# Performance work log

Hardware: AMD Instinct MI355X
Metric: run time of the kernel (lower is better)

Reference implementation:

```python
import jax, jax.numpy as jnp
import numpy as np

ATTN_K = 64
H = 256  # seq_hidden_size


def setup_inputs() -> dict:
    key = jax.random.key(0)
    ks = jax.random.split(key, 10)
    N, Q = 1000000, 256
    return {
        "question": jax.random.normal(ks[0], (Q,), jnp.float32),
        "score": jax.random.uniform(ks[1], (), jnp.float32),
        "questions": jax.random.normal(ks[2], (N, Q), jnp.float32),
        "hs": jax.random.normal(ks[3], (N, H), jnp.float32),
        "W_score": jax.random.normal(ks[4], (1, Q + H), jnp.float32) * 0.05,
        "b_score": jax.random.normal(ks[5], (1,), jnp.float32) * 0.05,
        "W_ih": jax.random.normal(ks[6], (3 * H, 2 * Q), jnp.float32) * 0.05,
        "W_hh": jax.random.normal(ks[7], (3 * H, H), jnp.float32) * 0.05,
        "b_ih": jax.random.normal(ks[8], (3 * H,), jnp.float32) * 0.05,
        "b_hh": jax.random.normal(ks[9], (3 * H,), jnp.float32) * 0.05,
    }


def reference(question, score, questions, hs, W_score, b_score, W_ih, W_hh, b_ih, b_hh):
    # Attention over history: dot-product scores, top-k, softmax-weighted sum.
    alpha = questions @ question                      # [N]
    vals, idx = jax.lax.top_k(alpha, ATTN_K)          # [k], [k]
    w = jax.nn.softmax(vals)                          # softmax over the k selected scores
    attn_h = w @ hs[idx]                              # [H] weighted gather-sum

    # Score head on [question ; attn_h]
    pred_v = jnp.concatenate([question, attn_h])      # [Q+H]
    pred = W_score @ pred_v + b_score                 # [1]

    # GRU input: question gated by correctness of score
    right = (score >= 0.5).astype(question.dtype)
    x = jnp.concatenate([question * right, question * (1.0 - right)])  # [2Q]

    # Single GRU step (PyTorch gate ordering: r, z, n)
    h = hs[-1]                                        # [H]
    gx = W_ih @ x + b_ih                              # [3H]
    gh = W_hh @ h + b_hh                              # [3H]
    xr, xz, xn = gx[:H], gx[H:2 * H], gx[2 * H:]
    hr, hz, hn = gh[:H], gh[H:2 * H], gh[2 * H:]
    r = jax.nn.sigmoid(xr + hr)
    z = jax.nn.sigmoid(xz + hz)
    n = jnp.tanh(xn + r * hn)
    h_new = (1.0 - z) * n + z * h                     # [H]
    return pred, h_new
```

## Files before the change

### kernel.cpp

```cpp
#include <hip/hip_runtime.h>
#include <math.h>

#define Q 256
#define H 256
#define ATTN_K 64
#define CAP 4096
#define HBINS 4096
#define NREP 8

typedef float f4 __attribute__((ext_vector_type(4)));

__device__ __forceinline__ unsigned f2k(float f) {
    unsigned u = __float_as_uint(f);
    return u ^ ((u & 0x80000000u) ? 0xFFFFFFFFu : 0x80000000u);
}

__global__ __launch_bounds__(256) void k_prep(const float* __restrict__ question,
                                              const float* __restrict__ score,
                                              const float* __restrict__ hs,
                                              const float* __restrict__ W_ih,
                                              const float* __restrict__ W_hh,
                                              const float* __restrict__ b_ih,
                                              const float* __restrict__ b_hh,
                                              float* __restrict__ gx, float* __restrict__ gh,
                                              unsigned* __restrict__ hist,
                                              unsigned* __restrict__ state, int N) {
    const int t = threadIdx.x;
    const int b = blockIdx.x;
    const int gid = b * 256 + t;
    if (gid < NREP * HBINS) hist[gid] = 0u;
    if (gid < 16) state[gid] = 0u;

    const int lane = t & 63;
    const int o = b * 4 + (t >> 6);
    if (o >= 3 * H) return;
    const int off = (score[0] >= 0.5f) ? 0 : Q;
    const float4 q = *reinterpret_cast<const float4*>(question + lane * 4);
    const float4 h = *reinterpret_cast<const float4*>(hs + (size_t)(N - 1) * H + lane * 4);
    const float4 wx = *reinterpret_cast<const float4*>(W_ih + (size_t)o * (2 * Q) + off + lane * 4);
    const float4 wh = *reinterpret_cast<const float4*>(W_hh + (size_t)o * H + lane * 4);
    float px = wx.x * q.x + wx.y * q.y + wx.z * q.z + wx.w * q.w;
    float ph = wh.x * h.x + wh.y * h.y + wh.z * h.z + wh.w * h.w;
#pragma unroll
    for (int d = 32; d > 0; d >>= 1) {
        px += __shfl_xor(px, d, 64);
        ph += __shfl_xor(ph, d, 64);
    }
    if (lane == 0) {
        gx[o] = px + b_ih[o];
        gh[o] = ph + b_hh[o];
    }
}

__global__ __launch_bounds__(256, 8) void k_main(const float* __restrict__ questions,
                                                 const float* __restrict__ question,
                                                 unsigned* __restrict__ hist,
                                                 float* __restrict__ alpha, int N) {
    __shared__ unsigned hb[HBINS];
    const int t = threadIdx.x;
    const int b = blockIdx.x;
#pragma unroll
    for (int j = 0; j < HBINS / 256; ++j) hb[t + j * 256] = 0u;
    __syncthreads();

    const int lane = t & 63;
    const int sub = lane & 15;
    const int rg  = lane >> 4;
    const int wid = b * 4 + (t >> 6);
    const int nw  = (gridDim.x * blockDim.x) >> 6;

    float4 q[4];
#pragma unroll
    for (int j = 0; j < 4; ++j)
        q[j] = *reinterpret_cast<const float4*>(question + j * 64 + sub * 4);

    const size_t stepRows = (size_t)nw * 8;
    const float* baseA = questions + ((size_t)wid * 8 + rg) * Q + sub * 4;
    for (size_t r0 = (size_t)wid * 8; r0 < (size_t)N; r0 += stepRows, baseA += stepRows * Q) {
        const int rA = (int)r0 + rg;
        const int rB = rA + 4;
        float pA = 0.f, pB = 0.f;
        if (rA < N) {
#pragma unroll
            for (int j = 0; j < 4; ++j) {
                f4 x = __builtin_nontemporal_load(reinterpret_cast<const f4*>(baseA + j * 64));
                pA = fmaf(x.x, q[j].x, fmaf(x.y, q[j].y, fmaf(x.z, q[j].z, fmaf(x.w, q[j].w, pA))));
            }
        }
        if (rB < N) {
#pragma unroll
            for (int j = 0; j < 4; ++j) {
                f4 x = __builtin_nontemporal_load(reinterpret_cast<const f4*>(baseA + 4 * Q + j * 64));
                pB = fmaf(x.x, q[j].x, fmaf(x.y, q[j].y, fmaf(x.z, q[j].z, fmaf(x.w, q[j].w, pB))));
            }
        }
#pragma unroll
        for (int d = 1; d < 16; d <<= 1) {
            pA += __shfl_xor(pA, d, 64);
            pB += __shfl_xor(pB, d, 64);
        }
        if (sub == 0) {
            if (rA < N) {
                alpha[rA] = pA;
                int rel = (int)(f2k(pA) >> 19) - 4096;
                if (rel >= 0) atomicAdd(&hb[rel], 1u);
            }
            if (rB < N) {
                alpha[rB] = pB;
                int rel = (int)(f2k(pB) >> 19) - 4096;
                if (rel >= 0) atomicAdd(&hb[rel], 1u);
            }
        }
    }

    __syncthreads();
    const unsigned rep = (unsigned)(b & (NREP - 1)) << 12;
#pragma unroll
    for (int j = 0; j < HBINS / 256; ++j) {
        unsigned v = hb[t + j * 256];
        if (v) atomicAdd(&hist[rep + t + j * 256], v);
    }
}

__global__ __launch_bounds__(256) void k_select(const float* __restrict__ alpha,
                                                const float* __restrict__ question,
                                                const float* __restrict__ hs,
                                                const float* __restrict__ W_score,
                                                const float* __restrict__ b_score,
                                                const unsigned* __restrict__ hist,
                                                unsigned* __restrict__ state,
                                                float* __restrict__ cval, int* __restrict__ cidx,
                                                const float* __restrict__ gx,
                                                const float* __restrict__ gh,
                                                float* __restrict__ out, int N) {
    __shared__ float lv[CAP];
    __shared__ int li[CAP];
    __shared__ float sw[ATTN_K];
    __shared__ int si[ATTN_K];
    __shared__ float red[256];
    __shared__ unsigned wsum[4];
    __shared__ int tau_sh;
    __shared__ int last_sh;
    const int t = threadIdx.x;
    const int lane = t & 63;
    const int w = t >> 6;

    unsigned c[16];
    {
        const int base16 = 4080 - 16 * t;
#pragma unroll
        for (int g = 0; g < 16; ++g) c[g] = 0u;
#pragma unroll
        for (int r = 0; r < NREP; ++r) {
            const uint4* h4 = reinterpret_cast<const uint4*>(hist + (r << 12) + base16);
#pragma unroll
            for (int k = 0; k < 4; ++k) {
                uint4 v = h4[k];
                c[4 * k + 0] += v.x; c[4 * k + 1] += v.y;
                c[4 * k + 2] += v.z; c[4 * k + 3] += v.w;
            }
        }
    }
    unsigned tsum = 0;
#pragma unroll
    for (int g = 0; g < 16; ++g) tsum += c[g];
    unsigned cum = tsum;
#pragma unroll
    for (int d = 1; d < 64; d <<= 1) {
        unsigned y = __shfl_up(cum, d, 64);
        if (lane >= d) cum += y;
    }
    if (lane == 63) wsum[w] = cum;
    __syncthreads();
    {
        unsigned add = 0;
        for (int i = 0; i < w; ++i) add += wsum[i];
        cum += add;
    }
    const unsigned before = cum - tsum;
    if (cum >= (unsigned)ATTN_K && before < (unsigned)ATTN_K) {
        unsigned acc = before;
        int taub = 4080 - 16 * t;
        for (int g = 15; g >= 0; --g) {
            acc += c[g];
            if (acc >= (unsigned)ATTN_K) { taub = 4080 - 16 * t + g; break; }
        }
        tau_sh = taub;
    }
    if (t == 255 && cum < (unsigned)ATTN_K) tau_sh = 0;
    __syncthreads();
    const int tau = tau_sh;

    {
        const int n4 = N >> 2;
        const int stride = gridDim.x * blockDim.x;
        const float4* a4 = reinterpret_cast<const float4*>(alpha);
        for (int i = blockIdx.x * blockDim.x + t; i < n4; i += stride) {
            float4 a = a4[i];
            float v[4] = {a.x, a.y, a.z, a.w};
#pragma unroll
            for (int j = 0; j < 4; ++j) {
                if ((int)(f2k(v[j]) >> 19) - 4096 >= tau) {
                    unsigned p = atomicAdd(&state[1], 1u);
                    if (p < CAP) { cval[p] = v[j]; cidx[p] = i * 4 + j; }
                }
            }
        }
        if (blockIdx.x == 0 && t < (N & 3)) {
            const int idx = (n4 << 2) + t;
            float v = alpha[idx];
            if ((int)(f2k(v) >> 19) - 4096 >= tau) {
                unsigned p = atomicAdd(&state[1], 1u);
                if (p < CAP) { cval[p] = v; cidx[p] = idx; }
            }
        }
    }

    if (t == 0) {
        __threadfence();
        last_sh = (atomicAdd(&state[2], 1u) == gridDim.x - 1) ? 1 : 0;
    }
    __syncthreads();
    if (!last_sh) return;
    __threadfence();

    const int C = min((int)state[1], CAP);
    for (int i = t; i < C; i += 256) { lv[i] = cval[i]; li[i] = cidx[i]; }
    __syncthreads();

    if (t < 64) {
        for (int k = 0; k < ATTN_K; ++k) {
            float bv = -INFINITY;
            int bi = 0x7fffffff;
            int bp = -1;
            for (int i = t; i < C; i += 64) {
                float v = lv[i];
                int id = li[i];
                if (v > bv || (v == bv && id < bi)) { bv = v; bi = id; bp = i; }
            }
#pragma unroll
            for (int d = 32; d > 0; d >>= 1) {
                float ov = __shfl_xor(bv, d, 64);
                int oi = __shfl_xor(bi, d, 64);
                int op = __shfl_xor(bp, d, 64);
                if (ov > bv || (ov == bv && oi < bi)) { bv = ov; bi = oi; bp = op; }
            }
            if (t == 0) {
                sw[k] = bv;
                si[k] = (bi == 0x7fffffff) ? 0 : bi;
                if (bp >= 0) lv[bp] = -INFINITY;
            }
        }
        float m = sw[0];
        float e = expf(sw[t] - m);
        float ssum = e;
#pragma unroll
        for (int d = 32; d > 0; d >>= 1) ssum += __shfl_xor(ssum, d, 64);
        sw[t] = e / ssum;
    }
    __syncthreads();

    float aj = 0.f;
    for (int k = 0; k < ATTN_K; ++k) {
        aj = fmaf(sw[k], hs[(size_t)si[k] * H + t], aj);
    }

    red[t] = W_score[t] * question[t] + W_score[Q + t] * aj;
    __syncthreads();
    for (int d = 128; d > 0; d >>= 1) {
        if (t < d) red[t] += red[t + d];
        __syncthreads();
    }
    if (t == 0) out[0] = red[0] + b_score[0];

    {
        float xr = gx[t], xz = gx[H + t], xn = gx[2 * H + t];
        float hr = gh[t], hz = gh[H + t], hn = gh[2 * H + t];
        float r = 1.f / (1.f + expf(-(xr + hr)));
        float z = 1.f / (1.f + expf(-(xz + hz)));
        float n = tanhf(xn + r * hn);
        float hprev = hs[(size_t)(N - 1) * H + t];
        out[1 + t] = (1.f - z) * n + z * hprev;
    }
}

extern "C" void kernel_launch(void* const* d_in, const int* in_sizes, int n_in,
                              void* d_out, int out_size, void* d_ws, size_t ws_size,
                              hipStream_t stream) {
    const float* question = (const float*)d_in[0];
    const float* score    = (const float*)d_in[1];
    const float* questions= (const float*)d_in[2];
    const float* hs       = (const float*)d_in[3];
    const float* W_score  = (const float*)d_in[4];
    const float* b_score  = (const float*)d_in[5];
    const float* W_ih     = (const float*)d_in[6];
    const float* W_hh     = (const float*)d_in[7];
    const float* b_ih     = (const float*)d_in[8];
    const float* b_hh     = (const float*)d_in[9];
    const int N = in_sizes[2] / Q;
    float* out = (float*)d_out;

    char* ws = (char*)d_ws;
    size_t off = 0;
    float* alpha = (float*)(ws + off); off += (size_t)N * sizeof(float);
    off = (off + 255) & ~(size_t)255;
    unsigned* hist = (unsigned*)(ws + off); off += (size_t)NREP * HBINS * sizeof(unsigned);
    unsigned* state = (unsigned*)(ws + off); off += 256;
    float* cval = (float*)(ws + off); off += (size_t)CAP * sizeof(float);
    int* cidx = (int*)(ws + off); off += (size_t)CAP * sizeof(int);
    float* gx = (float*)(ws + off); off += 3 * H * sizeof(float);
    float* gh = (float*)(ws + off); off += 3 * H * sizeof(float);

    k_prep<<<192, 256, 0, stream>>>(question, score, hs, W_ih, W_hh, b_ih, b_hh,
                                    gx, gh, hist, state, N);
    k_main<<<2048, 256, 0, stream>>>(questions, question, hist, alpha, N);
    k_select<<<512, 256, 0, stream>>>(alpha, question, hs, W_score, b_score, hist,
                                      state, cval, cidx, gx, gh, out, N);
}
```

Measured before the change: 243.3 us.

## Split histogram out of GEMV kernel and unroll four rows per wave

The streaming dot-product kernel no longer builds a shared-memory histogram, so it drops LDS allocation, the zeroing and merge syncs, and the per-row atomics. Each wave now handles 16 rows per iteration with four independent accumulators and no bounds checks, plus a separate tail loop, to raise memory-level parallelism. A new k_hist kernel re-reads alpha (4 MB) to build the histogram, which adds a launch and extra traffic in exchange for a leaner bandwidth-bound main loop.

After: 243.2 us. Within noise of the previous version (-0.1%).

```diff
diff --git a/kernel.cpp b/kernel.cpp
--- a/kernel.cpp
+++ b/kernel.cpp
@@ -52,21 +52,14 @@
     }
 }
 
-__global__ __launch_bounds__(256, 8) void k_main(const float* __restrict__ questions,
-                                                 const float* __restrict__ question,
-                                                 unsigned* __restrict__ hist,
-                                                 float* __restrict__ alpha, int N) {
-    __shared__ unsigned hb[HBINS];
+__global__ __launch_bounds__(256) void k_main(const float* __restrict__ questions,
+                                              const float* __restrict__ question,
+                                              float* __restrict__ alpha, int N) {
     const int t = threadIdx.x;
-    const int b = blockIdx.x;
-#pragma unroll
-    for (int j = 0; j < HBINS / 256; ++j) hb[t + j * 256] = 0u;
-    __syncthreads();
-
     const int lane = t & 63;
     const int sub = lane & 15;
     const int rg  = lane >> 4;
-    const int wid = b * 4 + (t >> 6);
+    const int wid = blockIdx.x * 4 + (t >> 6);
     const int nw  = (gridDim.x * blockDim.x) >> 6;
 
     float4 q[4];
@@ -74,51 +67,87 @@
     for (int j = 0; j < 4; ++j)
         q[j] = *reinterpret_cast<const float4*>(question + j * 64 + sub * 4);
 
-    const size_t stepRows = (size_t)nw * 8;
-    const float* baseA = questions + ((size_t)wid * 8 + rg) * Q + sub * 4;
-    for (size_t r0 = (size_t)wid * 8; r0 < (size_t)N; r0 += stepRows, baseA += stepRows * Q) {
-        const int rA = (int)r0 + rg;
-        const int rB = rA + 4;
-        float pA = 0.f, pB = 0.f;
-        if (rA < N) {
+    const int rowsPerIter = nw * 16;
+    const int B = N / rowsPerIter;
+    const float* base = questions + ((size_t)wid * 16 + rg) * Q + sub * 4;
+    for (int it = 0; it < B; ++it, base += (size_t)rowsPerIter * Q) {
+        float acc0 = 0.f, acc1 = 0.f, acc2 = 0.f, acc3 = 0.f;
+#pragma unroll
+        for (int j = 0; j < 4; ++j) {
+            f4 x0 = __builtin_nontemporal_load(reinterpret_cast<const f4*>(base + 0 * 4 * Q + j * 64));
+            f4 x1 = __builtin_nontemporal_load(reinterpret_cast<const f4*>(base + 1 * 4 * Q + j * 64));
+            f4 x2 = __builtin_nontemporal_load(reinterpret_cast<const f4*>(base + 2 * 4 * Q + j * 64));
+            f4 x3 = __builtin_nontemporal_load(reinterpret_cast<const f4*>(base + 3 * 4 * Q + j * 64));
+            acc0 = fmaf(x0.x, q[j].x, fmaf(x0.y, q[j].y, fmaf(x0.z, q[j].z, fmaf(x0.w, q[j].w, acc0))));
+            acc1 = fmaf(x1.x, q[j].x, fmaf(x1.y, q[j].y, fmaf(x1.z, q[j].z, fmaf(x1.w, q[j].w, acc1))));
+            acc2 = fmaf(x2.x, q[j].x, fmaf(x2.y, q[j].y, fmaf(x2.z, q[j].z, fmaf(x2.w, q[j].w, acc2))));
+            acc3 = fmaf(x3.x, q[j].x, fmaf(x3.y, q[j].y, fmaf(x3.z, q[j].z, fmaf(x3.w, q[j].w, acc3))));
+        }
+#pragma unroll
+        for (int d = 1; d < 16; d <<= 1) {
+            acc0 += __shfl_xor(acc0, d, 64);
+            acc1 += __shfl_xor(acc1, d, 64);
+            acc2 += __shfl_xor(acc2, d, 64);
+            acc3 += __shfl_xor(acc3, d, 64);
+        }
+        if (sub == 0) {
+            const size_t r0 = (size_t)it * rowsPerIter + (size_t)wid * 16 + rg;
+            alpha[r0]      = acc0;
+            alpha[r0 + 4]  = acc1;
+            alpha[r0 + 8]  = acc2;
+            alpha[r0 + 12] = acc3;
+        }
+    }
+
+    const int tailStart = B * rowsPerIter;
+    for (int g = wid; tailStart + g * 4 < N; g += nw) {
+        const int r = tailStart + g * 4 + rg;
+        float p = 0.f;
+        if (r < N) {
+            const float* row = questions + (size_t)r * Q + sub * 4;
 #pragma unroll
             for (int j = 0; j < 4; ++j) {
-                f4 x = __builtin_nontemporal_load(reinterpret_cast<const f4*>(baseA + j * 64));
-                pA = fmaf(x.x, q[j].x, fmaf(x.y, q[j].y, fmaf(x.z, q[j].z, fmaf(x.w, q[j].w, pA))));
-            }
-        }
-        if (rB < N) {
-#pragma unroll
-            for (int j = 0; j < 4; ++j) {
-                f4 x = __builtin_nontemporal_load(reinterpret_cast<const f4*>(baseA + 4 * Q + j * 64));
-                pB = fmaf(x.x, q[j].x, fmaf(x.y, q[j].y, fmaf(x.z, q[j].z, fmaf(x.w, q[j].w, pB))));
-            }
-        }
-#pragma unroll
-        for (int d = 1; d < 16; d <<= 1) {
-            pA += __shfl_xor(pA, d, 64);
-            pB += __shfl_xor(pB, d, 64);
-        }
-        if (sub == 0) {
-            if (rA < N) {
-                alpha[rA] = pA;
-                int rel = (int)(f2k(pA) >> 19) - 4096;
-                if (rel >= 0) atomicAdd(&hb[rel], 1u);
-            }
-            if (rB < N) {
-                alpha[rB] = pB;
-                int rel = (int)(f2k(pB) >> 19) - 4096;
-                if (rel >= 0) atomicAdd(&hb[rel], 1u);
-            }
-        }
-    }
-
-    __syncthreads();
-    const unsigned rep = (unsigned)(b & (NREP - 1)) << 12;
-#pragma unroll
-    for (int j = 0; j < HBINS / 256; ++j) {
-        unsigned v = hb[t + j * 256];
-        if (v) atomicAdd(&hist[rep + t + j * 256], v);
+                f4 x = __builtin_nontemporal_load(reinterpret_cast<const f4*>(row + j * 64));
+                p = fmaf(x.x, q[j].x, fmaf(x.y, q[j].y, fmaf(x.z, q[j].z, fmaf(x.w, q[j].w, p))));
+            }
+        }
+#pragma unroll
+        for (int d = 1; d < 16; d <<= 1) p += __shfl_xor(p, d, 64);
+        if (sub == 0 && r < N) alpha[r] = p;
+    }
+}
+
+__global__ __launch_bounds__(1024) void k_hist(const float* __restrict__ alpha,
+                                               unsigned* __restrict__ hist, int N) {
+    __shared__ unsigned hb[HBINS];
+    const int t = threadIdx.x;
+#pragma unroll
+    for (int j = 0; j < HBINS / 1024; ++j) hb[t + j * 1024] = 0u;
+    __syncthreads();
+
+    const int n4 = N >> 2;
+    const int stride = gridDim.x * blockDim.x;
+    const float4* a4 = reinterpret_cast<const float4*>(alpha);
+    for (int i = blockIdx.x * blockDim.x + t; i < n4; i += stride) {
+        float4 a = a4[i];
+        float v[4] = {a.x, a.y, a.z, a.w};
+#pragma unroll
+        for (int j = 0; j < 4; ++j) {
+            int rel = (int)(f2k(v[j]) >> 19) - 4096;
+            if (rel >= 0) atomicAdd(&hb[rel], 1u);
+        }
+    }
+    if (blockIdx.x == 0 && t < (N & 3)) {
+        float v = alpha[(n4 << 2) + t];
+        int rel = (int)(f2k(v) >> 19) - 4096;
+        if (rel >= 0) atomicAdd(&hb[rel], 1u);
+    }
+    __syncthreads();
+    const unsigned rep = (unsigned)(blockIdx.x & (NREP - 1)) << 12;
+#pragma unroll
+    for (int j = 0; j < HBINS / 1024; ++j) {
+        unsigned v = hb[t + j * 1024];
+        if (v) atomicAdd(&hist[rep + t + j * 1024], v);
     }
 }
 
@@ -313,7 +342,8 @@
 
     k_prep<<<192, 256, 0, stream>>>(question, score, hs, W_ih, W_hh, b_ih, b_hh,
                                     gx, gh, hist, state, N);
-    k_main<<<2048, 256, 0, stream>>>(questions, question, hist, alpha, N);
+    k_main<<<2048, 256, 0, stream>>>(questions, question, alpha, N);
+    k_hist<<<256, 1024, 0, stream>>>(alpha, hist, N);
     k_select<<<512, 256, 0, stream>>>(alpha, question, hs, W_score, b_score, hist,
                                       state, cval, cidx, gx, gh, out, N);
 }
```
